# Kernel tuning notes

Hardware: AMD Instinct MI355X
Metric: run time of the kernel (lower is better)

The kernel has to match this reference:

```python
import jax, jax.numpy as jnp
from jax import lax
import numpy as np

C_IN, C_OUT, G, K, PAD = 64, 128, 4, 3, 1
P = K * K
CG = C_IN // G
N, H, W = 8, 64, 64
LN_EPS = 1e-6
BN_EPS = 1e-5


def setup_inputs() -> dict:
    key = jax.random.key(0)
    ks = jax.random.split(key, 32)
    r = lambda i, shape, s=0.05: jax.random.normal(ks[i], shape, dtype=jnp.float32) * s
    return dict(
        x=jax.random.normal(ks[0], (N, C_IN, H, W), dtype=jnp.float32),
        reflectance=jax.random.uniform(ks[1], (N, 1, H, W), dtype=jnp.float32),
        gain_w1=r(2, (C_IN, C_IN // 4)), gain_b1=r(3, (C_IN // 4,)),
        gain_w2=r(4, (C_IN // 4, C_IN)), gain_b2=r(5, (C_IN,)),
        tap_w=r(6, (C_IN,)), tap_b=r(7, (C_IN,)),
        dw_w=r(8, (K, K, 1, C_IN)), dw_b=r(9, (C_IN,)),
        ln_g=jnp.ones((C_IN,), jnp.float32), ln_b=jnp.zeros((C_IN,), jnp.float32),
        inp_w=r(10, (C_IN, C_IN)), inp_b=r(11, (C_IN,)),
        off_w=r(12, (C_IN, G * P * 2), 0.02), off_b=r(13, (G * P * 2,), 0.02),
        mask_w=r(14, (C_IN, G * P), 0.02), mask_b=r(15, (G * P,), 0.02),
        outp_w=r(16, (C_IN, C_IN)), outp_b=r(17, (C_IN,)),
        conv_w=r(18, (C_IN, C_OUT)), conv_b=r(19, (C_OUT,)),
        bn1_g=jnp.ones((C_IN,), jnp.float32), bn1_b=jnp.zeros((C_IN,), jnp.float32),
        bn1_m=r(20, (C_IN,)),
        bn1_v=jax.random.uniform(ks[21], (C_IN,), minval=0.5, maxval=1.5),
        bn2_g=jnp.ones((C_OUT,), jnp.float32), bn2_b=jnp.zeros((C_OUT,), jnp.float32),
        bn2_m=r(22, (C_OUT,)),
        bn2_v=jax.random.uniform(ks[23], (C_OUT,), minval=0.5, maxval=1.5),
    )


def _bilinear_gather(xg, py, px):
    # xg: (N, Hp, Wp, G, CG); py/px: (N, H, W, G, P) absolute pixel coords
    # replicates F.grid_sample(mode='bilinear', padding_mode='zeros', align_corners=False)
    n_, Hp, Wp = xg.shape[0], xg.shape[1], xg.shape[2]
    y0 = jnp.floor(py)
    x0 = jnp.floor(px)
    wy = py - y0
    wx = px - x0
    nI = jnp.arange(n_).reshape(n_, 1, 1, 1, 1)
    gI = jnp.arange(G).reshape(1, 1, 1, G, 1)
    out = jnp.zeros(py.shape + (CG,), xg.dtype)
    for dy in (0, 1):
        for dx in (0, 1):
            yi = y0 + dy
            xi = x0 + dx
            w = (wy if dy else 1.0 - wy) * (wx if dx else 1.0 - wx)
            valid = (yi >= 0) & (yi < Hp) & (xi >= 0) & (xi < Wp)
            yc = jnp.clip(yi, 0, Hp - 1).astype(jnp.int32)
            xc = jnp.clip(xi, 0, Wp - 1).astype(jnp.int32)
            v = xg[nI, yc, xc, gI]  # (N, H, W, G, P, CG)
            out = out + (w * valid.astype(w.dtype))[..., None] * v
    return out


def reference(x, reflectance, gain_w1, gain_b1, gain_w2, gain_b2, tap_w, tap_b,
              dw_w, dw_b, ln_g, ln_b, inp_w, inp_b, off_w, off_b, mask_w, mask_b,
              outp_w, outp_b, conv_w, conv_b, bn1_g, bn1_b, bn1_m, bn1_v,
              bn2_g, bn2_b, bn2_m, bn2_v):
    n_, c_, h_, w_ = x.shape
    # ---- GainBlock (SE-style): x * sigmoid(mlp(avgpool(x))) + x ----
    pooled = x.mean(axis=(2, 3))                               # (N, C)
    g = jax.nn.relu(pooled @ gain_w1 + gain_b1)
    gain = jax.nn.sigmoid(g @ gain_w2 + gain_b2)               # (N, C)
    x = x * gain[:, :, None, None] + x
    # ---- ReflectiveFeedback: x + relu(conv1x1(reflectance)) ----
    refl = jax.nn.relu(reflectance * tap_w[None, :, None, None] + tap_b[None, :, None, None])
    x = x + refl                                               # (N, C, H, W)
    # ---- DCNv3 (pytorch version, group=4, k=3, pad=1, stride=1) ----
    xh = jnp.transpose(x, (0, 2, 3, 1))                        # NHWC
    xp = xh @ inp_w + inp_b                                    # input_proj
    dw = lax.conv_general_dilated(xh, dw_w, (1, 1), 'SAME',
                                  feature_group_count=c_,
                                  dimension_numbers=('NHWC', 'HWIO', 'NHWC')) + dw_b
    mu = dw.mean(-1, keepdims=True)
    var = dw.var(-1, keepdims=True)
    dw = ln_g * (dw - mu) * lax.rsqrt(var + LN_EPS) + ln_b     # LN channels_last
    dw = jax.nn.gelu(dw, approximate=False)
    offset = (dw @ off_w + off_b).reshape(n_, h_, w_, G, P, 2)
    mask = jax.nn.softmax((dw @ mask_w + mask_b).reshape(n_, h_, w_, G, P), axis=-1)
    # dcnv3_core: pad input, build reference + dilation grids (normalized by padded size)
    xpad = jnp.pad(xp, ((0, 0), (PAD, PAD), (PAD, PAD), (0, 0)))
    Hp, Wp = h_ + 2 * PAD, w_ + 2 * PAD
    ctr = (K - 1) // 2  # = (dilation*(k-1))//2 with dilation=1
    ref_y = (jnp.arange(h_, dtype=jnp.float32) + ctr + 0.5) / Hp
    ref_x = (jnp.arange(w_, dtype=jnp.float32) + ctr + 0.5) / Wp
    kk = jnp.arange(K, dtype=jnp.float32) - ctr                # [-1, 0, 1]
    gx = jnp.repeat(kk, K) / Wp                                # w-outer, h-inner order
    gy = jnp.tile(kk, K) / Hp
    loc_x = (ref_x[None, None, :, None, None] + gx[None, None, None, None, :]
             + offset[..., 0] / Wp)                            # (N,H,W,G,P)
    loc_y = (ref_y[None, :, None, None, None] + gy[None, None, None, None, :]
             + offset[..., 1] / Hp)
    px = loc_x * Wp - 0.5   # align_corners=False pixel coords
    py = loc_y * Hp - 0.5
    xg = xpad.reshape(n_, Hp, Wp, G, CG)
    samp = _bilinear_gather(xg, py, px)                        # (N,H,W,G,P,CG)
    dcn = (samp * mask[..., None]).sum(axis=4).reshape(n_, h_, w_, c_)
    dcn = dcn @ outp_w + outp_b                                # output_proj
    y = jnp.transpose(dcn, (0, 3, 1, 2))                       # back to NCHW
    # ---- bn1 -> relu -> conv1x1 -> bn2 -> relu (eval-mode BN) ----
    y = bn1_g[None, :, None, None] * (y - bn1_m[None, :, None, None]) \
        * lax.rsqrt(bn1_v[None, :, None, None] + BN_EPS) + bn1_b[None, :, None, None]
    y = jax.nn.relu(y)
    y = jnp.einsum('nchw,cd->ndhw', y, conv_w) + conv_b[None, :, None, None]
    y = bn2_g[None, :, None, None] * (y - bn2_m[None, :, None, None]) \
        * lax.rsqrt(bn2_v[None, :, None, None] + BN_EPS) + bn2_b[None, :, None, None]
    return jax.nn.relu(y)
```

## Files before the change

kernel.cpp:

```cpp
#include <hip/hip_runtime.h>
#include <math.h>


__global__ __launch_bounds__(256) void k_pool(const float* x, float* pooled) {
    __shared__ float red[256];
    int b = blockIdx.x;
    int nc = ((b & 7) << 6) | (b >> 3);
    const float4* p4 = reinterpret_cast<const float4*>(x + (size_t)nc * 4096);
    float s = 0.f;
    for (int i = threadIdx.x; i < 1024; i += 256) {
        float4 v = p4[i];
        s += v.x + v.y + v.z + v.w;
    }
    red[threadIdx.x] = s;
    __syncthreads();
    for (int o = 128; o > 0; o >>= 1) {
        if (threadIdx.x < o) red[threadIdx.x] += red[threadIdx.x + o];
        __syncthreads();
    }
    if (threadIdx.x == 0) pooled[nc] = red[0] * (1.f / 4096.f);
}

__global__ __launch_bounds__(128) void k_xsproj(
        const float* x, const float* refl,
        const float* tap_w, const float* tap_b,
        const float* pooled,
        const float* gw1, const float* gb1,
        const float* gw2, const float* gb2,
        const float* inp_w, const float* inp_b,
        float* xs, float* xpad) {
    __shared__ float tile[64 * 9];
    __shared__ float xsrow[8][68];
    __shared__ float hid[16];
    __shared__ float gain[64];
    __shared__ float rrow[8];
    int b = blockIdx.x;
    int n = b & 7, rem = b >> 3;
    int h = rem >> 3, wc = rem & 7, w0 = wc * 8;
    int nh = n * 64 + h;
    int tid = threadIdx.x;

    {
        int c = tid >> 1, wq = (tid & 1) * 4;
        const float4 v = *reinterpret_cast<const float4*>(
            &x[(((size_t)(n * 64 + c)) * 64 + h) * 64 + w0 + wq]);
        tile[c * 9 + wq + 0] = v.x;
        tile[c * 9 + wq + 1] = v.y;
        tile[c * 9 + wq + 2] = v.z;
        tile[c * 9 + wq + 3] = v.w;
    }
    if (tid < 8) rrow[tid] = refl[n * 4096 + h * 64 + w0 + tid];
    if (tid >= 64 && tid < 80) {
        int j = tid - 64;
        float s = gb1[j];
        for (int c = 0; c < 64; ++c) s += pooled[n * 64 + c] * gw1[c * 16 + j];
        hid[j] = fmaxf(s, 0.f);
    }
    __syncthreads();

    if (tid < 64) {
        float s = gb2[tid];
        #pragma unroll
        for (int j = 0; j < 16; ++j) s += hid[j] * gw2[j * 64 + tid];
        gain[tid] = 1.f + 1.f / (1.f + __expf(-s));
    }
    __syncthreads();

    {
        int c = tid & 63, wg = tid >> 6;
        float gv = gain[c], tw = tap_w[c], tb = tap_b[c];
        #pragma unroll
        for (int k = 0; k < 4; ++k) {
            int w = wg * 4 + k;
            float r = fmaxf(rrow[w] * tw + tb, 0.f);
            float v = tile[c * 9 + w] * gv + r;
            xsrow[w][c] = v;
            xs[(((size_t)nh) * 64 + w0 + w) * 64 + c] = v;
        }
    }
    __syncthreads();

    {
        int co = tid & 63, wg = tid >> 6;
        float acc[4];
        float bv = inp_b[co];
        #pragma unroll
        for (int i = 0; i < 4; ++i) acc[i] = bv;
        for (int c4 = 0; c4 < 64; c4 += 4) {
            float q0 = inp_w[(c4 + 0) * 64 + co];
            float q1 = inp_w[(c4 + 1) * 64 + co];
            float q2 = inp_w[(c4 + 2) * 64 + co];
            float q3 = inp_w[(c4 + 3) * 64 + co];
            #pragma unroll
            for (int i = 0; i < 4; ++i) {
                float4 d = *reinterpret_cast<const float4*>(&xsrow[wg * 4 + i][c4]);
                acc[i] += d.x * q0 + d.y * q1 + d.z * q2 + d.w * q3;
            }
        }
        const size_t rowb = (((size_t)n * 66) + (h + 1)) * 66;
        #pragma unroll
        for (int i = 0; i < 4; ++i) {
            int w = wg * 4 + i;
            xpad[(rowb + (w0 + w + 1)) * 64 + co] = acc[i];
        }
        if (wc == 0 && tid < 64) xpad[rowb * 64 + tid] = 0.f;
        if (wc == 7 && tid < 64) xpad[(rowb + 65) * 64 + tid] = 0.f;
        if (h == 0 || h == 63) {
            const size_t rb = (((size_t)n * 66) + (h == 0 ? 0 : 65)) * 66;
            for (int i = tid; i < 512; i += 128) {
                int q = 1 + w0 + (i >> 6), cc = i & 63;
                xpad[(rb + q) * 64 + cc] = 0.f;
            }
            if (wc == 0 && tid < 64) xpad[rb * 64 + tid] = 0.f;
            if (wc == 7 && tid < 64) xpad[(rb + 65) * 64 + tid] = 0.f;
        }
    }
}

#define WAVE_FENCE() asm volatile("s_waitcnt lgkmcnt(0)" ::: "memory")

__global__ __launch_bounds__(128, 4) void k_dwsamp(const float* xs, const float* xpad,
                       const float* dw_w, const float* dw_b,
                       const float* ln_g, const float* ln_b,
                       const float* off_w, const float* off_b,
                       const float* mask_w, const float* mask_b,
                       const float* outp_w, const float* outp_b,
                       const float* bn1_g, const float* bn1_b,
                       const float* bn1_m, const float* bn1_v,
                       const float* conv_w, const float* conv_b,
                       const float* bn2_g, const float* bn2_b,
                       const float* bn2_m, const float* bn2_v,
                       float* out) {
    __shared__ float smem[2816];

    int tid = threadIdx.x;
    int lane = tid & 63, wv = tid >> 6;
    float*  chunk = smem + wv * 1408;
    int4*   sad   = reinterpret_cast<int4*>(chunk);
    float*  dwr   = chunk;
    float4* swt   = reinterpret_cast<float4*>(chunk + 576);
    float*  dcnl  = chunk + 1152;
    float*  mlog  = chunk + 1152;

    int b = blockIdx.x;
    int n = b & 7;
    int pos0 = (b >> 3) * 8 + wv * 4;
    int h = pos0 >> 6, w0 = pos0 & 63;

    {
        float dwk[9];
        #pragma unroll
        for (int k = 0; k < 9; ++k) dwk[k] = dw_w[k * 64 + lane];
        float s[4];
        float bvv = dw_b[lane];
        #pragma unroll
        for (int p = 0; p < 4; ++p) s[p] = bvv;
        for (int ky = 0; ky < 3; ++ky) {
            int y = h + ky - 1;
            if (y < 0 || y > 63) continue;
            const float* xrow = xs + ((size_t)(n * 64 + y)) * 4096;
            float v[6];
            #pragma unroll
            for (int dx = 0; dx < 6; ++dx) {
                int x2 = w0 - 1 + dx;
                v[dx] = (x2 >= 0 && x2 <= 63) ? xrow[x2 * 64 + lane] : 0.f;
            }
            float k0 = dwk[ky * 3 + 0], k1 = dwk[ky * 3 + 1], k2 = dwk[ky * 3 + 2];
            #pragma unroll
            for (int p = 0; p < 4; ++p)
                s[p] += v[p] * k0 + v[p + 1] * k1 + v[p + 2] * k2;
        }
        float lngv = ln_g[lane], lnbv = ln_b[lane];
        #pragma unroll
        for (int p = 0; p < 4; ++p) {
            float sv = s[p];
            float sum = sv, sq = sv * sv;
            #pragma unroll
            for (int o = 32; o > 0; o >>= 1) {
                sum += __shfl_xor(sum, o, 64);
                sq  += __shfl_xor(sq,  o, 64);
            }
            float mu = sum * (1.f / 64.f);
            float var = sq * (1.f / 64.f) - mu * mu;
            float nrm = (sv - mu) * rsqrtf(var + 1e-6f) * lngv + lnbv;
            dwr[p * 64 + lane] = 0.5f * nrm * (1.f + erff(nrm * 0.70710678118654752f));
        }
    }
    WAVE_FENCE();

    float a0[4], a1[4];
    {
        int jb = lane * 2;
        const float* wptr;
        int stride;
        float b0 = 0.f, b1 = 0.f;
        if (lane < 36)      { wptr = off_w + jb;         stride = 72; b0 = off_b[jb];       b1 = off_b[jb + 1]; }
        else if (lane < 54) { wptr = mask_w + (jb - 72); stride = 36; b0 = mask_b[jb - 72]; b1 = mask_b[jb - 71]; }
        else                { wptr = off_w;              stride = 0; }
        #pragma unroll
        for (int p = 0; p < 4; ++p) { a0[p] = b0; a1[p] = b1; }
        for (int c4 = 0; c4 < 64; c4 += 4) {
            float4 d0 = *reinterpret_cast<const float4*>(&dwr[0 * 64 + c4]);
            float4 d1 = *reinterpret_cast<const float4*>(&dwr[1 * 64 + c4]);
            float4 d2 = *reinterpret_cast<const float4*>(&dwr[2 * 64 + c4]);
            float4 d3 = *reinterpret_cast<const float4*>(&dwr[3 * 64 + c4]);
            float dk0[4] = {d0.x, d0.y, d0.z, d0.w};
            float dk1[4] = {d1.x, d1.y, d1.z, d1.w};
            float dk2[4] = {d2.x, d2.y, d2.z, d2.w};
            float dk3[4] = {d3.x, d3.y, d3.z, d3.w};
            #pragma unroll
            for (int k = 0; k < 4; ++k) {
                float2 w2 = *reinterpret_cast<const float2*>(wptr);
                wptr += stride;
                a0[0] += dk0[k] * w2.x;  a1[0] += dk0[k] * w2.y;
                a0[1] += dk1[k] * w2.x;  a1[1] += dk1[k] * w2.y;
                a0[2] += dk2[k] * w2.x;  a1[2] += dk2[k] * w2.y;
                a0[3] += dk3[k] * w2.x;  a1[3] += dk3[k] * w2.y;
            }
        }
        if (lane >= 36 && lane < 54) {
            int jm = lane * 2 - 72;
            #pragma unroll
            for (int p = 0; p < 4; ++p) {
                mlog[p * 40 + jm]     = a0[p];
                mlog[p * 40 + jm + 1] = a1[p];
            }
        }
    }
    WAVE_FENCE();

    if (lane < 36) {
        int g = lane / 9, pp = lane - g * 9;
        #pragma unroll
        for (int p = 0; p < 4; ++p) {
            const float* lrow = &mlog[p * 40 + g * 9];
            float m = lrow[0];
            #pragma unroll
            for (int k = 1; k < 9; ++k) m = fmaxf(m, lrow[k]);
            float ssum = 0.f, ek = 0.f;
            #pragma unroll
            for (int k = 0; k < 9; ++k) {
                float e = __expf(lrow[k] - m);
                ssum += e;
                if (k == pp) ek = e;
            }
            float mk = ek / ssum;
            float px = (float)((w0 + p) + (pp / 3)) + a0[p];
            float py = (float)(h + (pp % 3)) + a1[p];
            float x0f = floorf(px), y0f = floorf(py);
            float wx = px - x0f, wy = py - y0f;
            int x0 = (int)x0f, y0 = (int)y0f;
            int x1 = x0 + 1, y1 = y0 + 1;
            int xc0 = min(max(x0, 0), 65), xc1 = min(max(x1, 0), 65);
            int yc0 = min(max(y0, 0), 65), yc1 = min(max(y1, 0), 65);
            float vx0 = (x0 >= 0 && x0 < 66) ? 1.f : 0.f;
            float vx1 = (x1 >= 0 && x1 < 66) ? 1.f : 0.f;
            float vy0 = (y0 >= 0 && y0 < 66) ? 1.f : 0.f;
            float vy1 = (y1 >= 0 && y1 < 66) ? 1.f : 0.f;
            float wx0 = (1.f - wx) * vx0, wx1 = wx * vx1;
            float wy0 = (1.f - wy) * vy0, wy1 = wy * vy1;
            swt[p * 36 + lane] = make_float4(mk * wy0 * wx0, mk * wy0 * wx1,
                                             mk * wy1 * wx0, mk * wy1 * wx1);
            sad[p * 36 + lane] = make_int4((yc0 * 66 + xc0) * 64, (yc0 * 66 + xc1) * 64,
                                           (yc1 * 66 + xc0) * 64, (yc1 * 66 + xc1) * 64);
        }
    }
    WAVE_FENCE();

    {
        int gb = (lane >> 4) * 9;
        const float* xpn = xpad + (size_t)n * 66 * 66 * 64;
        #pragma unroll
        for (int p = 0; p < 4; ++p) {
            float t0[9], t1[9], t2[9], t3[9];
            #pragma unroll
            for (int pp = 0; pp < 9; ++pp) {
                int4 a = sad[p * 36 + gb + pp];
                t0[pp] = xpn[a.x + lane];
                t1[pp] = xpn[a.y + lane];
                t2[pp] = xpn[a.z + lane];
                t3[pp] = xpn[a.w + lane];
            }
            float acc = 0.f;
            #pragma unroll
            for (int pp = 0; pp < 9; ++pp) {
                float4 cw = swt[p * 36 + gb + pp];
                acc += cw.x * t0[pp] + cw.y * t1[pp]
                     + cw.z * t2[pp] + cw.w * t3[pp];
            }
            dcnl[p * 64 + lane] = acc;
        }
    }
    WAVE_FENCE();

    {
        float ob = outp_b[lane];
        float s0 = ob, s1 = ob, s2 = ob, s3 = ob;
        for (int c4 = 0; c4 < 64; c4 += 4) {
            float w0v = outp_w[(c4 + 0) * 64 + lane];
            float w1v = outp_w[(c4 + 1) * 64 + lane];
            float w2v = outp_w[(c4 + 2) * 64 + lane];
            float w3v = outp_w[(c4 + 3) * 64 + lane];
            float4 d0 = *reinterpret_cast<const float4*>(&dcnl[0 * 64 + c4]);
            float4 d1 = *reinterpret_cast<const float4*>(&dcnl[1 * 64 + c4]);
            float4 d2 = *reinterpret_cast<const float4*>(&dcnl[2 * 64 + c4]);
            float4 d3 = *reinterpret_cast<const float4*>(&dcnl[3 * 64 + c4]);
            s0 += d0.x * w0v + d0.y * w1v + d0.z * w2v + d0.w * w3v;
            s1 += d1.x * w0v + d1.y * w1v + d1.z * w2v + d1.w * w3v;
            s2 += d2.x * w0v + d2.y * w1v + d2.z * w2v + d2.w * w3v;
            s3 += d3.x * w0v + d3.y * w1v + d3.z * w2v + d3.w * w3v;
        }
        float sc = bn1_g[lane] * rsqrtf(bn1_v[lane] + 1e-5f);
        float sh = bn1_b[lane] - sc * bn1_m[lane];
        WAVE_FENCE();
        dcnl[0 * 64 + lane] = fmaxf(sc * s0 + sh, 0.f);
        dcnl[1 * 64 + lane] = fmaxf(sc * s1 + sh, 0.f);
        dcnl[2 * 64 + lane] = fmaxf(sc * s2 + sh, 0.f);
        dcnl[3 * 64 + lane] = fmaxf(sc * s3 + sh, 0.f);
    }
    WAVE_FENCE();

    {
        float accA[4], accB[4];
        #pragma unroll
        for (int p = 0; p < 4; ++p) { accA[p] = 0.f; accB[p] = 0.f; }
        for (int c4 = 0; c4 < 64; c4 += 4) {
            float4 d0 = *reinterpret_cast<const float4*>(&dcnl[0 * 64 + c4]);
            float4 d1 = *reinterpret_cast<const float4*>(&dcnl[1 * 64 + c4]);
            float4 d2 = *reinterpret_cast<const float4*>(&dcnl[2 * 64 + c4]);
            float4 d3 = *reinterpret_cast<const float4*>(&dcnl[3 * 64 + c4]);
            float dk0[4] = {d0.x, d0.y, d0.z, d0.w};
            float dk1[4] = {d1.x, d1.y, d1.z, d1.w};
            float dk2[4] = {d2.x, d2.y, d2.z, d2.w};
            float dk3[4] = {d3.x, d3.y, d3.z, d3.w};
            #pragma unroll
            for (int k = 0; k < 4; ++k) {
                float wa = conv_w[(c4 + k) * 128 + lane];
                float wb = conv_w[(c4 + k) * 128 + 64 + lane];
                accA[0] += dk0[k] * wa;  accB[0] += dk0[k] * wb;
                accA[1] += dk1[k] * wa;  accB[1] += dk1[k] * wb;
                accA[2] += dk2[k] * wa;  accB[2] += dk2[k] * wb;
                accA[3] += dk3[k] * wa;  accB[3] += dk3[k] * wb;
            }
        }
        int dA = lane, dB = lane + 64;
        float scA = bn2_g[dA] * rsqrtf(bn2_v[dA] + 1e-5f);
        float shA = scA * (conv_b[dA] - bn2_m[dA]) + bn2_b[dA];
        float scB = bn2_g[dB] * rsqrtf(bn2_v[dB] + 1e-5f);
        float shB = scB * (conv_b[dB] - bn2_m[dB]) + bn2_b[dB];
        float4 rA, rB;
        rA.x = fmaxf(scA * accA[0] + shA, 0.f);
        rA.y = fmaxf(scA * accA[1] + shA, 0.f);
        rA.z = fmaxf(scA * accA[2] + shA, 0.f);
        rA.w = fmaxf(scA * accA[3] + shA, 0.f);
        rB.x = fmaxf(scB * accB[0] + shB, 0.f);
        rB.y = fmaxf(scB * accB[1] + shB, 0.f);
        rB.z = fmaxf(scB * accB[2] + shB, 0.f);
        rB.w = fmaxf(scB * accB[3] + shB, 0.f);
        size_t oA = (((size_t)(n * 128 + dA)) * 64 + h) * 64 + w0;
        size_t oB = (((size_t)(n * 128 + dB)) * 64 + h) * 64 + w0;
        *reinterpret_cast<float4*>(out + oA) = rA;
        *reinterpret_cast<float4*>(out + oB) = rB;
    }
}

extern "C" void kernel_launch(void* const* d_in, const int* in_sizes, int n_in,
                              void* d_out, int out_size, void* d_ws, size_t ws_size,
                              hipStream_t stream) {
    const float* x      = (const float*)d_in[0];
    const float* refl   = (const float*)d_in[1];
    const float* gw1    = (const float*)d_in[2];
    const float* gb1    = (const float*)d_in[3];
    const float* gw2    = (const float*)d_in[4];
    const float* gb2    = (const float*)d_in[5];
    const float* tap_w  = (const float*)d_in[6];
    const float* tap_b  = (const float*)d_in[7];
    const float* dw_w   = (const float*)d_in[8];
    const float* dw_b   = (const float*)d_in[9];
    const float* ln_g   = (const float*)d_in[10];
    const float* ln_b   = (const float*)d_in[11];
    const float* inp_w  = (const float*)d_in[12];
    const float* inp_b  = (const float*)d_in[13];
    const float* off_w  = (const float*)d_in[14];
    const float* off_b  = (const float*)d_in[15];
    const float* mask_w = (const float*)d_in[16];
    const float* mask_b = (const float*)d_in[17];
    const float* outp_w = (const float*)d_in[18];
    const float* outp_b = (const float*)d_in[19];
    const float* conv_w = (const float*)d_in[20];
    const float* conv_b = (const float*)d_in[21];
    const float* bn1_g  = (const float*)d_in[22];
    const float* bn1_b  = (const float*)d_in[23];
    const float* bn1_m  = (const float*)d_in[24];
    const float* bn1_v  = (const float*)d_in[25];
    const float* bn2_g  = (const float*)d_in[26];
    const float* bn2_b  = (const float*)d_in[27];
    const float* bn2_m  = (const float*)d_in[28];
    const float* bn2_v  = (const float*)d_in[29];

    float* ws     = (float*)d_ws;
    float* pooled = ws;
    float* xs     = ws + 512;
    float* xpad   = xs + 2097152;

    k_pool<<<512, 256, 0, stream>>>(x, pooled);
    k_xsproj<<<4096, 128, 0, stream>>>(x, refl, tap_w, tap_b, pooled,
                                       gw1, gb1, gw2, gb2, inp_w, inp_b, xs, xpad);
    k_dwsamp<<<4096, 128, 0, stream>>>(xs, xpad, dw_w, dw_b, ln_g, ln_b,
                                       off_w, off_b, mask_w, mask_b,
                                       outp_w, outp_b, bn1_g, bn1_b, bn1_m, bn1_v,
                                       conv_w, conv_b, bn2_g, bn2_b, bn2_m, bn2_v,
                                       (float*)d_out);
}
```

Baseline: 188.7 us.

## Hoist channel-gain MLP into separate kernel and make xsproj wave-independent

After: 193.5 us. +2.5%, slower.

```diff
diff --git a/kernel.cpp b/kernel.cpp
--- a/kernel.cpp
+++ b/kernel.cpp
@@ -1,6 +1,8 @@
 #include <hip/hip_runtime.h>
 #include <math.h>
 
+
+#define WAVE_FENCE() asm volatile("s_waitcnt lgkmcnt(0)" ::: "memory")
 
 __global__ __launch_bounds__(256) void k_pool(const float* x, float* pooled) {
     __shared__ float red[256];
@@ -21,103 +23,103 @@
     if (threadIdx.x == 0) pooled[nc] = red[0] * (1.f / 4096.f);
 }
 
+__global__ __launch_bounds__(64) void k_gain(const float* pooled,
+        const float* gw1, const float* gb1,
+        const float* gw2, const float* gb2,
+        float* gain) {
+    int n = blockIdx.x;
+    int lane = threadIdx.x;
+    float pv = pooled[n * 64 + lane];
+    float part[16];
+    const float4* g4 = reinterpret_cast<const float4*>(gw1 + lane * 16);
+    #pragma unroll
+    for (int q = 0; q < 4; ++q) {
+        float4 v = g4[q];
+        part[q * 4 + 0] = pv * v.x;
+        part[q * 4 + 1] = pv * v.y;
+        part[q * 4 + 2] = pv * v.z;
+        part[q * 4 + 3] = pv * v.w;
+    }
+    #pragma unroll
+    for (int o = 32; o > 0; o >>= 1) {
+        #pragma unroll
+        for (int j = 0; j < 16; ++j) part[j] += __shfl_xor(part[j], o, 64);
+    }
+    float acc = gb2[lane];
+    #pragma unroll
+    for (int j = 0; j < 16; ++j) {
+        float hj = fmaxf(part[j] + gb1[j], 0.f);
+        acc += hj * gw2[j * 64 + lane];
+    }
+    gain[n * 64 + lane] = 1.f + 1.f / (1.f + __expf(-acc));
+}
+
 __global__ __launch_bounds__(128) void k_xsproj(
         const float* x, const float* refl,
         const float* tap_w, const float* tap_b,
-        const float* pooled,
-        const float* gw1, const float* gb1,
-        const float* gw2, const float* gb2,
+        const float* gain,
         const float* inp_w, const float* inp_b,
         float* xs, float* xpad) {
-    __shared__ float tile[64 * 9];
-    __shared__ float xsrow[8][68];
-    __shared__ float hid[16];
-    __shared__ float gain[64];
-    __shared__ float rrow[8];
+    __shared__ float xsrow[2][4][64];
+    int tid = threadIdx.x;
+    int lane = tid & 63, wv = tid >> 6;
     int b = blockIdx.x;
     int n = b & 7, rem = b >> 3;
-    int h = rem >> 3, wc = rem & 7, w0 = wc * 8;
+    int h = rem >> 3, wc = rem & 7;
+    int w0 = wc * 8 + wv * 4;
     int nh = n * 64 + h;
-    int tid = threadIdx.x;
-
-    {
-        int c = tid >> 1, wq = (tid & 1) * 4;
-        const float4 v = *reinterpret_cast<const float4*>(
-            &x[(((size_t)(n * 64 + c)) * 64 + h) * 64 + w0 + wq]);
-        tile[c * 9 + wq + 0] = v.x;
-        tile[c * 9 + wq + 1] = v.y;
-        tile[c * 9 + wq + 2] = v.z;
-        tile[c * 9 + wq + 3] = v.w;
-    }
-    if (tid < 8) rrow[tid] = refl[n * 4096 + h * 64 + w0 + tid];
-    if (tid >= 64 && tid < 80) {
-        int j = tid - 64;
-        float s = gb1[j];
-        for (int c = 0; c < 64; ++c) s += pooled[n * 64 + c] * gw1[c * 16 + j];
-        hid[j] = fmaxf(s, 0.f);
-    }
-    __syncthreads();
-
-    if (tid < 64) {
-        float s = gb2[tid];
-        #pragma unroll
-        for (int j = 0; j < 16; ++j) s += hid[j] * gw2[j * 64 + tid];
-        gain[tid] = 1.f + 1.f / (1.f + __expf(-s));
-    }
-    __syncthreads();
-
-    {
-        int c = tid & 63, wg = tid >> 6;
-        float gv = gain[c], tw = tap_w[c], tb = tap_b[c];
-        #pragma unroll
-        for (int k = 0; k < 4; ++k) {
-            int w = wg * 4 + k;
-            float r = fmaxf(rrow[w] * tw + tb, 0.f);
-            float v = tile[c * 9 + w] * gv + r;
-            xsrow[w][c] = v;
-            xs[(((size_t)nh) * 64 + w0 + w) * 64 + c] = v;
-        }
-    }
-    __syncthreads();
-
-    {
-        int co = tid & 63, wg = tid >> 6;
+    float (*xr)[64] = xsrow[wv];
+
+    {
+        float4 xv = *reinterpret_cast<const float4*>(
+            &x[(((size_t)(n * 64 + lane)) * 64 + h) * 64 + w0]);
+        float gv = gain[n * 64 + lane];
+        float tw = tap_w[lane], tb = tap_b[lane];
+        const float* rp = refl + n * 4096 + h * 64 + w0;
+        float xvv[4] = {xv.x, xv.y, xv.z, xv.w};
+        #pragma unroll
+        for (int i = 0; i < 4; ++i) {
+            float r = fmaxf(rp[i] * tw + tb, 0.f);
+            float v = xvv[i] * gv + r;
+            xr[i][lane] = v;
+            xs[(((size_t)nh) * 64 + w0 + i) * 64 + lane] = v;
+        }
+    }
+    WAVE_FENCE();
+
+    {
         float acc[4];
-        float bv = inp_b[co];
+        float bv = inp_b[lane];
         #pragma unroll
         for (int i = 0; i < 4; ++i) acc[i] = bv;
+        #pragma unroll
         for (int c4 = 0; c4 < 64; c4 += 4) {
-            float q0 = inp_w[(c4 + 0) * 64 + co];
-            float q1 = inp_w[(c4 + 1) * 64 + co];
-            float q2 = inp_w[(c4 + 2) * 64 + co];
-            float q3 = inp_w[(c4 + 3) * 64 + co];
+            float q0 = inp_w[(c4 + 0) * 64 + lane];
+            float q1 = inp_w[(c4 + 1) * 64 + lane];
+            float q2 = inp_w[(c4 + 2) * 64 + lane];
+            float q3 = inp_w[(c4 + 3) * 64 + lane];
             #pragma unroll
             for (int i = 0; i < 4; ++i) {
-                float4 d = *reinterpret_cast<const float4*>(&xsrow[wg * 4 + i][c4]);
+                float4 d = *reinterpret_cast<const float4*>(&xr[i][c4]);
                 acc[i] += d.x * q0 + d.y * q1 + d.z * q2 + d.w * q3;
             }
         }
         const size_t rowb = (((size_t)n * 66) + (h + 1)) * 66;
         #pragma unroll
-        for (int i = 0; i < 4; ++i) {
-            int w = wg * 4 + i;
-            xpad[(rowb + (w0 + w + 1)) * 64 + co] = acc[i];
-        }
-        if (wc == 0 && tid < 64) xpad[rowb * 64 + tid] = 0.f;
-        if (wc == 7 && tid < 64) xpad[(rowb + 65) * 64 + tid] = 0.f;
+        for (int i = 0; i < 4; ++i)
+            xpad[(rowb + (w0 + i + 1)) * 64 + lane] = acc[i];
+        if (w0 == 0)  xpad[rowb * 64 + lane] = 0.f;
+        if (w0 == 60) xpad[(rowb + 65) * 64 + lane] = 0.f;
         if (h == 0 || h == 63) {
             const size_t rb = (((size_t)n * 66) + (h == 0 ? 0 : 65)) * 66;
-            for (int i = tid; i < 512; i += 128) {
-                int q = 1 + w0 + (i >> 6), cc = i & 63;
-                xpad[(rb + q) * 64 + cc] = 0.f;
-            }
-            if (wc == 0 && tid < 64) xpad[rb * 64 + tid] = 0.f;
-            if (wc == 7 && tid < 64) xpad[(rb + 65) * 64 + tid] = 0.f;
+            #pragma unroll
+            for (int i = 0; i < 4; ++i)
+                xpad[(rb + 1 + w0 + i) * 64 + lane] = 0.f;
+            if (w0 == 0)  xpad[rb * 64 + lane] = 0.f;
+            if (w0 == 60) xpad[(rb + 65) * 64 + lane] = 0.f;
         }
     }
 }
-
-#define WAVE_FENCE() asm volatile("s_waitcnt lgkmcnt(0)" ::: "memory")
 
 __global__ __launch_bounds__(128, 4) void k_dwsamp(const float* xs, const float* xpad,
                        const float* dw_w, const float* dw_b,
@@ -400,12 +402,14 @@
 
     float* ws     = (float*)d_ws;
     float* pooled = ws;
-    float* xs     = ws + 512;
+    float* gaing  = ws + 512;
+    float* xs     = ws + 1024;
     float* xpad   = xs + 2097152;
 
     k_pool<<<512, 256, 0, stream>>>(x, pooled);
-    k_xsproj<<<4096, 128, 0, stream>>>(x, refl, tap_w, tap_b, pooled,
-                                       gw1, gb1, gw2, gb2, inp_w, inp_b, xs, xpad);
+    k_gain<<<8, 64, 0, stream>>>(pooled, gw1, gb1, gw2, gb2, gaing);
+    k_xsproj<<<4096, 128, 0, stream>>>(x, refl, tap_w, tap_b, gaing,
+                                       inp_w, inp_b, xs, xpad);
     k_dwsamp<<<4096, 128, 0, stream>>>(xs, xpad, dw_w, dw_b, ln_g, ln_b,
                                        off_w, off_b, mask_w, mask_b,
                                        outp_w, outp_b, bn1_g, bn1_b, bn1_m, bn1_v,
```
